# Kernel optimization log

Hardware: AMD Instinct MI355X
Metric: run time of the kernel (lower is better)

Reference implementation:

```python
import jax, jax.numpy as jnp
import numpy as np

N = 100000          # num_nodes
E_TYPES = 5         # num_edge_type
N_EDGES = 500000    # edges per relation type
W_IN = 256
W_OUT = 128         # args.node_dim
C = 2               # args.num_channels
L = 2               # args.num_layers
NUM_CLASS = 3
BETA = 0.1


def _glorot(k, sh):
    lim = np.sqrt(6.0 / (sh[-2] + sh[-1]))
    return jax.random.uniform(k, sh, jnp.float32, -lim, lim)


def setup_inputs() -> dict:
    key = jax.random.key(0)
    ks = jax.random.split(key, 8)
    edge_index = jax.random.randint(ks[0], (E_TYPES, 2, N_EDGES), 0, N)
    edge_value = jax.random.uniform(ks[1], (E_TYPES, N_EDGES), dtype=jnp.float32)
    X = jax.random.normal(ks[2], (N, W_IN), dtype=jnp.float32)
    Ws = _glorot(ks[3], (C, W_IN, W_OUT))                      # GCNConv weights per channel
    conv_w = jax.random.normal(ks[4], (L, C, E_TYPES), dtype=jnp.float32) * 0.1  # FastGTConv weights
    lin1_w = _glorot(ks[5], (C * W_OUT, W_OUT))
    lin1_b = jnp.zeros((W_OUT,), jnp.float32)
    lin2_w = _glorot(ks[6], (W_OUT, NUM_CLASS))
    lin2_b = jnp.zeros((NUM_CLASS,), jnp.float32)
    return dict(edge_index=edge_index, edge_value=edge_value, X=X, Ws=Ws,
                conv_w=conv_w, lin1_w=lin1_w, lin1_b=lin1_b,
                lin2_w=lin2_w, lin2_b=lin2_b, num_nodes=N)


def reference(edge_index, edge_value, X, Ws, conv_w, lin1_w, lin1_b, lin2_w, lin2_b, num_nodes):
    # channel-wise input projections: X_[c] = X @ Ws[c]   -> [C, N, d]
    X_ = jnp.einsum('nf,cfo->cno', X, Ws)
    H = X_
    for l in range(L):
        filt = jax.nn.softmax(conv_w[l], axis=1)  # [C, E] per-channel softmax over edge types
        H_new = jnp.zeros_like(H)
        for j in range(E_TYPES):
            row, col = edge_index[j, 0], edge_index[j, 1]
            # sparse A_j @ H per channel: gather cols, weight by edge value, scatter-add rows
            msg = H[:, col, :] * edge_value[j][None, :, None]          # [C, Ej, d]
            agg = jax.vmap(lambda m: jax.ops.segment_sum(m, row, num_segments=num_nodes))(msg)
            H_new = H_new + filt[:, j][:, None, None] * agg
        # NOTE: source's `H = H + init_H` is Python list concat -> unused entries; no residual.
        H = H_new
    Hrelu = jax.nn.relu(BETA * X_ + (1.0 - BETA) * H)                  # [C, N, d]
    H_ = jnp.concatenate([Hrelu[c] for c in range(C)], axis=1)         # channel_agg='concat'
    H_ = H_ @ lin1_w + lin1_b                                          # [N, d]
    return H_ @ lin2_w + lin2_b                                        # [N, num_class]
```

## Files before the change

### kernel.cpp

```cpp
#include <hip/hip_runtime.h>

#define NN   100000
#define ETY  5
#define NE   500000
#define WIN  256
#define WOUT 128
#define CCH  2
#define LAY  2
#define NCLS 3

#define NTOT   (ETY * NE)
#define BSHIFT 7
#define BNODES 128
#define NBUCK  ((NN + BNODES - 1) / BNODES)
#define BCAP   4096
#define ACHUNK 8192

typedef __attribute__((ext_vector_type(8))) short bf16x8;
typedef __attribute__((ext_vector_type(4))) float f32x4;

__device__ __forceinline__ unsigned short f2bf(float f) {
    union { float f; unsigned u; } v; v.f = f;
    unsigned u = v.u + 0x7FFFu + ((v.u >> 16) & 1u);
    return (unsigned short)(u >> 16);
}
__device__ __forceinline__ float bf2f(unsigned short u) {
    union { unsigned u; float f; } v; v.u = ((unsigned)u) << 16;
    return v.f;
}

__device__ __forceinline__ bf16x8 pack8(float4 a, float4 b) {
    bf16x8 r;
    r[0] = (short)f2bf(a.x); r[1] = (short)f2bf(a.y);
    r[2] = (short)f2bf(a.z); r[3] = (short)f2bf(a.w);
    r[4] = (short)f2bf(b.x); r[5] = (short)f2bf(b.y);
    r[6] = (short)f2bf(b.z); r[7] = (short)f2bf(b.w);
    return r;
}

__global__ void filt_kernel(const float* __restrict__ conv_w, float* __restrict__ filt) {
    int g = threadIdx.x;
    if (g < LAY * CCH) {
        float m = -1e30f;
        for (int j = 0; j < ETY; ++j) m = fmaxf(m, conv_w[g * ETY + j]);
        float e[ETY], s = 0.f;
        for (int j = 0; j < ETY; ++j) { e[j] = __expf(conv_w[g * ETY + j] - m); s += e[j]; }
        float inv = 1.f / s;
        for (int j = 0; j < ETY; ++j) filt[g * ETY + j] = e[j] * inv;
    }
}

__global__ void wconv_kernel(const float* __restrict__ Ws, const float* __restrict__ w1,
                             unsigned short* __restrict__ Wsb, unsigned short* __restrict__ w1b) {
    int i = blockIdx.x * 256 + threadIdx.x;
    if (i < CCH * WOUT * WIN) {
        int c = i / (WOUT * WIN);
        int r = i - c * WOUT * WIN;
        int n = r / WIN;
        int k = r - n * WIN;
        Wsb[i] = f2bf(Ws[((size_t)c * WIN + k) * WOUT + n]);
    }
    if (i < WOUT * (CCH * WOUT)) {
        int n = i / (CCH * WOUT);
        int k = i - n * (CCH * WOUT);
        w1b[i] = f2bf(w1[(size_t)k * WOUT + n]);
    }
}

__global__ void proj_kernel(const float* __restrict__ X, const unsigned short* __restrict__ Wsb,
                            unsigned short* __restrict__ Xpb) {
    const int tid  = threadIdx.x;
    const int lane = tid & 63;
    const int wv   = tid >> 6;
    const int row0 = blockIdx.x * 64 + wv * 16;
    const int ar   = lane & 15;
    const int kg   = lane >> 4;
    int arow = row0 + ar; if (arow >= NN) arow = NN - 1;
    const float* xrow = X + (size_t)arow * WIN + kg * 8;

    f32x4 acc[2][8];
#pragma unroll
    for (int c = 0; c < 2; ++c)
#pragma unroll
        for (int nt = 0; nt < 8; ++nt) acc[c][nt] = (f32x4){0.f, 0.f, 0.f, 0.f};

#pragma unroll
    for (int kk = 0; kk < 8; ++kk) {
        float4 a0 = *(const float4*)(xrow + kk * 32);
        float4 a1 = *(const float4*)(xrow + kk * 32 + 4);
        bf16x8 af = pack8(a0, a1);
#pragma unroll
        for (int c = 0; c < 2; ++c)
#pragma unroll
            for (int nt = 0; nt < 8; ++nt) {
                const bf16x8 bfm = *(const bf16x8*)(Wsb + (size_t)c * WOUT * WIN +
                                                    (size_t)(nt * 16 + ar) * WIN + kk * 32 + kg * 8);
                acc[c][nt] = __builtin_amdgcn_mfma_f32_16x16x32_bf16(af, bfm, acc[c][nt], 0, 0, 0);
            }
    }
#pragma unroll
    for (int nt = 0; nt < 8; ++nt) {
#pragma unroll
        for (int q = 0; q < 4; ++q) {
            int r = row0 + kg * 4 + q;
            if (r < NN) {
                int col = nt * 16 + ar;
                ushort2 w;
                w.x = f2bf(acc[0][nt][q]);
                w.y = f2bf(acc[1][nt][q]);
                *(ushort2*)(Xpb + (size_t)r * (WOUT * CCH) + col * 2) = w;
            }
        }
    }
}

__global__ void __launch_bounds__(256) bucket_kernel(const int* __restrict__ edge_index,
                                                     const float* __restrict__ edge_value,
                                                     int* __restrict__ bcur, int2* __restrict__ rec) {
    __shared__ int hist[NBUCK];
    __shared__ int start_s[NBUCK];
    const int tid = threadIdx.x;
    const int i0 = blockIdx.x * ACHUNK;
    int i1 = i0 + ACHUNK; if (i1 > NTOT) i1 = NTOT;
    for (int t = tid; t < NBUCK; t += 256) hist[t] = 0;
    __syncthreads();
    for (int i = i0 + tid; i < i1; i += 256) {
        int j = i / NE; int e = i - j * NE;
        int row = edge_index[(size_t)j * 2 * NE + e];
        atomicAdd(&hist[row >> BSHIFT], 1);
    }
    __syncthreads();
    for (int t = tid; t < NBUCK; t += 256) {
        int h = hist[t];
        start_s[t] = h ? atomicAdd(&bcur[t], h) : 0;
        hist[t] = 0;
    }
    __syncthreads();
    for (int i = i0 + tid; i < i1; i += 256) {
        int j = i / NE; int e = i - j * NE;
        int row = edge_index[(size_t)j * 2 * NE + e];
        int col = edge_index[(size_t)j * 2 * NE + NE + e];
        int bk = row >> BSHIFT;
        int p = start_s[bk] + atomicAdd(&hist[bk], 1);
        if (p < BCAP)
            rec[(size_t)bk * BCAP + p] =
                make_int2(col | (j << 17) | ((row & (BNODES - 1)) << 20), __float_as_int(edge_value[i]));
    }
}

__global__ void __launch_bounds__(256) sortb_kernel(const int2* __restrict__ rec,
                                                    const int* __restrict__ bcur,
                                                    const float* __restrict__ filt,
                                                    int* __restrict__ colF, float2* __restrict__ wv0F,
                                                    float2* __restrict__ wv1F, int* __restrict__ baseF,
                                                    int* __restrict__ cntF) {
    __shared__ int nh[BNODES];
    __shared__ int nb[BNODES + 1];
    __shared__ int2 srec[BCAP];
    __shared__ float fl[4 * ETY];
    const int b = blockIdx.x;
    const int tid = threadIdx.x;
    int cnt = bcur[b]; if (cnt > BCAP) cnt = BCAP;
    if (tid < BNODES) nh[tid] = 0;
    if (tid < 4 * ETY) fl[tid] = filt[tid];
    __syncthreads();
    const int2* rb = rec + (size_t)b * BCAP;
    for (int k = tid; k < cnt; k += 256) {
        int r = (rb[k].x >> 20) & (BNODES - 1);
        atomicAdd(&nh[r], 1);
    }
    __syncthreads();
    if (tid < BNODES) nb[tid + 1] = nh[tid];
    if (tid == 0) nb[0] = 0;
    __syncthreads();
    for (int off = 1; off < BNODES; off <<= 1) {
        int v = 0;
        if (tid < BNODES) { v = nb[tid + 1]; if (tid + 1 > off) v += nb[tid + 1 - off]; }
        __syncthreads();
        if (tid < BNODES) nb[tid + 1] = v;
        __syncthreads();
    }
    if (tid < BNODES) nh[tid] = 0;
    __syncthreads();
    for (int k = tid; k < cnt; k += 256) {
        int2 R = rb[k];
        int r = (R.x >> 20) & (BNODES - 1);
        int p = nb[r] + atomicAdd(&nh[r], 1);
        srec[p] = R;
    }
    __syncthreads();
    const size_t g0 = (size_t)b * BCAP;
    for (int k = tid; k < cnt; k += 256) {
        int2 R = srec[k];
        int col = R.x & 0x1FFFF;
        int j = (R.x >> 17) & 7;
        float ev = __int_as_float(R.y);
        colF[g0 + k] = col;
        wv0F[g0 + k] = make_float2(fl[j] * ev, fl[ETY + j] * ev);
        wv1F[g0 + k] = make_float2(fl[2 * ETY + j] * ev, fl[3 * ETY + j] * ev);
    }
    if (tid < BNODES) {
        int n = b * BNODES + tid;
        if (n < NN) {
            baseF[n] = (int)(g0 + nb[tid]);
            cntF[n]  = nb[tid + 1] - nb[tid];
        }
    }
}

__global__ void gather_kernel(const unsigned short* __restrict__ Hin, unsigned short* __restrict__ Hnew,
                              const int* __restrict__ base, const int* __restrict__ cnt,
                              const int* __restrict__ colF, const float2* __restrict__ wv) {
    const int lane = threadIdx.x & 63;
    const int wib  = threadIdx.x >> 6;
    int n0 = blockIdx.x * 4 + wib;
    if (n0 >= NN) return;
    const int n = __builtin_amdgcn_readfirstlane(n0);
    const unsigned short* hp = Hin + lane * 4;
    float a0 = 0.f, a1 = 0.f, a2 = 0.f, a3 = 0.f;
    const int kb = __builtin_amdgcn_readfirstlane(base[n]);
    const int ce = __builtin_amdgcn_readfirstlane(cnt[n]);
    const int e = kb + ce;
    for (int k = kb; k < e; k += 8) {
        int cs[8];
#pragma unroll
        for (int u = 0; u < 8; ++u) {
            int ku = k + u;
            cs[u] = colF[ku < e ? ku : e - 1];
        }
        ushort4 vs[8];
#pragma unroll
        for (int u = 0; u < 8; ++u)
            vs[u] = *(const ushort4*)(hp + (size_t)cs[u] * (WOUT * CCH));
        float2 ws[8];
#pragma unroll
        for (int u = 0; u < 8; ++u) {
            int ku = k + u;
            float2 w = wv[ku < e ? ku : e - 1];
            if (ku >= e) { w.x = 0.f; w.y = 0.f; }
            ws[u] = w;
        }
#pragma unroll
        for (int u = 0; u < 8; ++u) {
            a0 = fmaf(ws[u].x, bf2f(vs[u].x), a0);
            a1 = fmaf(ws[u].y, bf2f(vs[u].y), a1);
            a2 = fmaf(ws[u].x, bf2f(vs[u].z), a2);
            a3 = fmaf(ws[u].y, bf2f(vs[u].w), a3);
        }
    }
    ushort4 r4;
    r4.x = f2bf(a0); r4.y = f2bf(a1); r4.z = f2bf(a2); r4.w = f2bf(a3);
    *(ushort4*)(Hnew + (size_t)n * (WOUT * CCH) + lane * 4) = r4;
}

__global__ void lin_kernel(const unsigned short* __restrict__ Xpb, const unsigned short* __restrict__ Hb,
                           const unsigned short* __restrict__ w1b, const float* __restrict__ b1,
                           const float* __restrict__ w2, const float* __restrict__ b2,
                           float* __restrict__ out) {
    const int tid  = threadIdx.x;
    const int lane = tid & 63;
    const int wv   = tid >> 6;
    const int row0 = blockIdx.x * 64 + wv * 16;
    const int ar   = lane & 15;
    const int kg   = lane >> 4;
    int arow = row0 + ar; if (arow >= NN) arow = NN - 1;
    const unsigned short* xr = Xpb + (size_t)arow * (WOUT * CCH);
    const unsigned short* hr = Hb  + (size_t)arow * (WOUT * CCH);

    f32x4 acc[8];
#pragma unroll
    for (int nt = 0; nt < 8; ++nt) acc[nt] = (f32x4){0.f, 0.f, 0.f, 0.f};

    bf16x8 af1s[4];
#pragma unroll
    for (int kk = 0; kk < 4; ++kk) {
        const int d = kk * 32 + kg * 8;
        bf16x8 af0, af1;
#pragma unroll
        for (int t = 0; t < 4; ++t) {
            ushort4 xu = *(const ushort4*)(xr + 2 * d + 4 * t);
            ushort4 hu = *(const ushort4*)(hr + 2 * d + 4 * t);
            float v00 = fmaxf(0.1f * bf2f(xu.x) + 0.9f * bf2f(hu.x), 0.f);
            float v01 = fmaxf(0.1f * bf2f(xu.y) + 0.9f * bf2f(hu.y), 0.f);
            float v10 = fmaxf(0.1f * bf2f(xu.z) + 0.9f * bf2f(hu.z), 0.f);
            float v11 = fmaxf(0.1f * bf2f(xu.w) + 0.9f * bf2f(hu.w), 0.f);
            af0[2 * t]     = (short)f2bf(v00);
            af0[2 * t + 1] = (short)f2bf(v10);
            af1[2 * t]     = (short)f2bf(v01);
            af1[2 * t + 1] = (short)f2bf(v11);
        }
        af1s[kk] = af1;
        const int k0 = kk * 32 + kg * 8;
#pragma unroll
        for (int nt = 0; nt < 8; ++nt) {
            const bf16x8 bfm = *(const bf16x8*)(w1b + (size_t)(nt * 16 + ar) * (CCH * WOUT) + k0);
            acc[nt] = __builtin_amdgcn_mfma_f32_16x16x32_bf16(af0, bfm, acc[nt], 0, 0, 0);
        }
    }
#pragma unroll
    for (int kk = 4; kk < 8; ++kk) {
        const int k0 = kk * 32 + kg * 8;
        const bf16x8 af = af1s[kk - 4];
#pragma unroll
        for (int nt = 0; nt < 8; ++nt) {
            const bf16x8 bfm = *(const bf16x8*)(w1b + (size_t)(nt * 16 + ar) * (CCH * WOUT) + k0);
            acc[nt] = __builtin_amdgcn_mfma_f32_16x16x32_bf16(af, bfm, acc[nt], 0, 0, 0);
        }
    }

    float b1v[8], w2v[8][NCLS];
#pragma unroll
    for (int nt = 0; nt < 8; ++nt) {
        int col = nt * 16 + ar;
        b1v[nt] = b1[col];
#pragma unroll
        for (int m = 0; m < NCLS; ++m) w2v[nt][m] = w2[col * NCLS + m];
    }
#pragma unroll
    for (int q = 0; q < 4; ++q) {
        float pm[NCLS] = {0.f, 0.f, 0.f};
#pragma unroll
        for (int nt = 0; nt < 8; ++nt) {
            float h = acc[nt][q] + b1v[nt];
#pragma unroll
            for (int m = 0; m < NCLS; ++m) pm[m] = fmaf(h, w2v[nt][m], pm[m]);
        }
#pragma unroll
        for (int m = 0; m < NCLS; ++m) {
            pm[m] += __shfl_xor(pm[m], 1);
            pm[m] += __shfl_xor(pm[m], 2);
            pm[m] += __shfl_xor(pm[m], 4);
            pm[m] += __shfl_xor(pm[m], 8);
        }
        int r = row0 + kg * 4 + q;
        if (ar == 0 && r < NN) {
            out[(size_t)r * NCLS + 0] = pm[0] + b2[0];
            out[(size_t)r * NCLS + 1] = pm[1] + b2[1];
            out[(size_t)r * NCLS + 2] = pm[2] + b2[2];
        }
    }
}

extern "C" void kernel_launch(void* const* d_in, const int* in_sizes, int n_in,
                              void* d_out, int out_size, void* d_ws, size_t ws_size,
                              hipStream_t stream) {
    const int*   edge_index = (const int*)d_in[0];
    const float* edge_value = (const float*)d_in[1];
    const float* X          = (const float*)d_in[2];
    const float* Ws         = (const float*)d_in[3];
    const float* conv_w     = (const float*)d_in[4];
    const float* lin1_w     = (const float*)d_in[5];
    const float* lin1_b     = (const float*)d_in[6];
    const float* lin2_w     = (const float*)d_in[7];
    const float* lin2_b     = (const float*)d_in[8];
    float* out = (float*)d_out;

    const size_t CNU  = (size_t)NN * WOUT * CCH;
    const size_t SLOT = (size_t)NBUCK * BCAP;
    unsigned short* Xpb = (unsigned short*)d_ws;
    unsigned short* Ab  = Xpb + CNU;
    unsigned short* Bb  = Ab + CNU;
    float*  filt = (float*)(Bb + CNU);
    int*    bcur = (int*)(filt + 32);
    int*    baseF = bcur + NBUCK;
    int*    cntF  = baseF + NN;
    int2*   rec   = (int2*)(cntF + NN);
    int*    colF  = (int*)(rec + SLOT);
    float2* wv0F  = (float2*)(colF + SLOT);
    float2* wv1F  = wv0F + SLOT;
    unsigned short* Wsb = (unsigned short*)(wv1F + SLOT);
    unsigned short* w1b = Wsb + (size_t)CCH * WOUT * WIN;

    hipMemsetAsync(bcur, 0, NBUCK * sizeof(int), stream);

    filt_kernel<<<1, 64, 0, stream>>>(conv_w, filt);
    wconv_kernel<<<(CCH * WOUT * WIN + 255) / 256, 256, 0, stream>>>(Ws, lin1_w, Wsb, w1b);

    proj_kernel<<<(NN + 63) / 64, 256, 0, stream>>>(X, Wsb, Xpb);

    bucket_kernel<<<(NTOT + ACHUNK - 1) / ACHUNK, 256, 0, stream>>>(edge_index, edge_value, bcur, rec);
    sortb_kernel<<<NBUCK, 256, 0, stream>>>(rec, bcur, filt, colF, wv0F, wv1F, baseF, cntF);

    const int gblocks = (NN + 3) / 4;
    gather_kernel<<<gblocks, 256, 0, stream>>>(Xpb, Ab, baseF, cntF, colF, wv0F);
    gather_kernel<<<gblocks, 256, 0, stream>>>(Ab, Bb, baseF, cntF, colF, wv1F);

    lin_kernel<<<(NN + 63) / 64, 256, 0, stream>>>(Xpb, Bb, w1b, lin1_b, lin2_w, lin2_b, out);
}
```

Baseline: 653.0 us.

## Pack edge column and bf16 weights into one int2 record for gather

Sort output now stores each edge as an int2 holding the column index and two bf16 channel weights, replacing separate column and float2 weight arrays. The gather loop then issues one record load per edge instead of two, which cuts index-stream traffic. The bucket kernel gets a 2D grid indexed by edge type, removing per-element divides, and the filter softmax is folded into the weight-conversion kernel to save a launch. Weights lose precision by being rounded to bf16.

```diff
diff --git a/kernel.cpp b/kernel.cpp
--- a/kernel.cpp
+++ b/kernel.cpp
@@ -15,6 +15,7 @@
 #define NBUCK  ((NN + BNODES - 1) / BNODES)
 #define BCAP   4096
 #define ACHUNK 8192
+#define ABLK   ((NE + ACHUNK - 1) / ACHUNK)
 
 typedef __attribute__((ext_vector_type(8))) short bf16x8;
 typedef __attribute__((ext_vector_type(4))) float f32x4;
@@ -38,9 +39,13 @@
     return r;
 }
 
-__global__ void filt_kernel(const float* __restrict__ conv_w, float* __restrict__ filt) {
-    int g = threadIdx.x;
-    if (g < LAY * CCH) {
+__global__ void wconv_kernel(const float* __restrict__ Ws, const float* __restrict__ w1,
+                             const float* __restrict__ conv_w,
+                             unsigned short* __restrict__ Wsb, unsigned short* __restrict__ w1b,
+                             float* __restrict__ filt) {
+    int i = blockIdx.x * 256 + threadIdx.x;
+    if (i < LAY * CCH) {
+        int g = i;
         float m = -1e30f;
         for (int j = 0; j < ETY; ++j) m = fmaxf(m, conv_w[g * ETY + j]);
         float e[ETY], s = 0.f;
@@ -48,11 +53,6 @@
         float inv = 1.f / s;
         for (int j = 0; j < ETY; ++j) filt[g * ETY + j] = e[j] * inv;
     }
-}
-
-__global__ void wconv_kernel(const float* __restrict__ Ws, const float* __restrict__ w1,
-                             unsigned short* __restrict__ Wsb, unsigned short* __restrict__ w1b) {
-    int i = blockIdx.x * 256 + threadIdx.x;
     if (i < CCH * WOUT * WIN) {
         int c = i / (WOUT * WIN);
         int r = i - c * WOUT * WIN;
@@ -120,15 +120,16 @@
     __shared__ int hist[NBUCK];
     __shared__ int start_s[NBUCK];
     const int tid = threadIdx.x;
+    const int j = blockIdx.y;
     const int i0 = blockIdx.x * ACHUNK;
-    int i1 = i0 + ACHUNK; if (i1 > NTOT) i1 = NTOT;
+    int i1 = i0 + ACHUNK; if (i1 > NE) i1 = NE;
+    const int* rows = edge_index + (size_t)j * 2 * NE;
+    const int* cols = rows + NE;
+    const float* evs = edge_value + (size_t)j * NE;
     for (int t = tid; t < NBUCK; t += 256) hist[t] = 0;
     __syncthreads();
-    for (int i = i0 + tid; i < i1; i += 256) {
-        int j = i / NE; int e = i - j * NE;
-        int row = edge_index[(size_t)j * 2 * NE + e];
-        atomicAdd(&hist[row >> BSHIFT], 1);
-    }
+    for (int i = i0 + tid; i < i1; i += 256)
+        atomicAdd(&hist[rows[i] >> BSHIFT], 1);
     __syncthreads();
     for (int t = tid; t < NBUCK; t += 256) {
         int h = hist[t];
@@ -137,23 +138,21 @@
     }
     __syncthreads();
     for (int i = i0 + tid; i < i1; i += 256) {
-        int j = i / NE; int e = i - j * NE;
-        int row = edge_index[(size_t)j * 2 * NE + e];
-        int col = edge_index[(size_t)j * 2 * NE + NE + e];
+        int row = rows[i];
+        int col = cols[i];
         int bk = row >> BSHIFT;
         int p = start_s[bk] + atomicAdd(&hist[bk], 1);
         if (p < BCAP)
             rec[(size_t)bk * BCAP + p] =
-                make_int2(col | (j << 17) | ((row & (BNODES - 1)) << 20), __float_as_int(edge_value[i]));
+                make_int2(col | (j << 17) | ((row & (BNODES - 1)) << 20), __float_as_int(evs[i]));
     }
 }
 
 __global__ void __launch_bounds__(256) sortb_kernel(const int2* __restrict__ rec,
                                                     const int* __restrict__ bcur,
                                                     const float* __restrict__ filt,
-                                                    int* __restrict__ colF, float2* __restrict__ wv0F,
-                                                    float2* __restrict__ wv1F, int* __restrict__ baseF,
-                                                    int* __restrict__ cntF) {
+                                                    int2* __restrict__ ew0F, int2* __restrict__ ew1F,
+                                                    int* __restrict__ baseF, int* __restrict__ cntF) {
     __shared__ int nh[BNODES];
     __shared__ int nb[BNODES + 1];
     __shared__ int2 srec[BCAP];
@@ -195,9 +194,13 @@
         int col = R.x & 0x1FFFF;
         int j = (R.x >> 17) & 7;
         float ev = __int_as_float(R.y);
-        colF[g0 + k] = col;
-        wv0F[g0 + k] = make_float2(fl[j] * ev, fl[ETY + j] * ev);
-        wv1F[g0 + k] = make_float2(fl[2 * ETY + j] * ev, fl[3 * ETY + j] * ev);
+        int2 E0, E1;
+        E0.x = col;
+        E0.y = (int)((unsigned)f2bf(fl[j] * ev) | ((unsigned)f2bf(fl[ETY + j] * ev) << 16));
+        E1.x = col;
+        E1.y = (int)((unsigned)f2bf(fl[2 * ETY + j] * ev) | ((unsigned)f2bf(fl[3 * ETY + j] * ev) << 16));
+        ew0F[g0 + k] = E0;
+        ew1F[g0 + k] = E1;
     }
     if (tid < BNODES) {
         int n = b * BNODES + tid;
@@ -210,7 +213,7 @@
 
 __global__ void gather_kernel(const unsigned short* __restrict__ Hin, unsigned short* __restrict__ Hnew,
                               const int* __restrict__ base, const int* __restrict__ cnt,
-                              const int* __restrict__ colF, const float2* __restrict__ wv) {
+                              const int2* __restrict__ ewF) {
     const int lane = threadIdx.x & 63;
     const int wib  = threadIdx.x >> 6;
     int n0 = blockIdx.x * 4 + wib;
@@ -222,30 +225,25 @@
     const int ce = __builtin_amdgcn_readfirstlane(cnt[n]);
     const int e = kb + ce;
     for (int k = kb; k < e; k += 8) {
-        int cs[8];
+        int2 es[8];
 #pragma unroll
         for (int u = 0; u < 8; ++u) {
             int ku = k + u;
-            cs[u] = colF[ku < e ? ku : e - 1];
+            es[u] = ewF[ku < e ? ku : e - 1];
         }
         ushort4 vs[8];
 #pragma unroll
         for (int u = 0; u < 8; ++u)
-            vs[u] = *(const ushort4*)(hp + (size_t)cs[u] * (WOUT * CCH));
-        float2 ws[8];
+            vs[u] = *(const ushort4*)(hp + (size_t)es[u].x * (WOUT * CCH));
 #pragma unroll
         for (int u = 0; u < 8; ++u) {
-            int ku = k + u;
-            float2 w = wv[ku < e ? ku : e - 1];
-            if (ku >= e) { w.x = 0.f; w.y = 0.f; }
-            ws[u] = w;
-        }
-#pragma unroll
-        for (int u = 0; u < 8; ++u) {
-            a0 = fmaf(ws[u].x, bf2f(vs[u].x), a0);
-            a1 = fmaf(ws[u].y, bf2f(vs[u].y), a1);
-            a2 = fmaf(ws[u].x, bf2f(vs[u].z), a2);
-            a3 = fmaf(ws[u].y, bf2f(vs[u].w), a3);
+            float w0 = bf2f((unsigned short)(es[u].y & 0xFFFF));
+            float w1 = bf2f((unsigned short)(((unsigned)es[u].y) >> 16));
+            if (k + u >= e) { w0 = 0.f; w1 = 0.f; }
+            a0 = fmaf(w0, bf2f(vs[u].x), a0);
+            a1 = fmaf(w1, bf2f(vs[u].y), a1);
+            a2 = fmaf(w0, bf2f(vs[u].z), a2);
+            a3 = fmaf(w1, bf2f(vs[u].w), a3);
         }
     }
     ushort4 r4;
@@ -360,30 +358,29 @@
     unsigned short* Xpb = (unsigned short*)d_ws;
     unsigned short* Ab  = Xpb + CNU;
     unsigned short* Bb  = Ab + CNU;
-    float*  filt = (float*)(Bb + CNU);
-    int*    bcur = (int*)(filt + 32);
+    float*  filt  = (float*)(Bb + CNU);
+    int*    bcur  = (int*)(filt + 32);
     int*    baseF = bcur + NBUCK;
     int*    cntF  = baseF + NN;
     int2*   rec   = (int2*)(cntF + NN);
-    int*    colF  = (int*)(rec + SLOT);
-    float2* wv0F  = (float2*)(colF + SLOT);
-    float2* wv1F  = wv0F + SLOT;
-    unsigned short* Wsb = (unsigned short*)(wv1F + SLOT);
+    int2*   ew0F  = rec + SLOT;
+    int2*   ew1F  = ew0F + SLOT;
+    unsigned short* Wsb = (unsigned short*)(ew1F + SLOT);
     unsigned short* w1b = Wsb + (size_t)CCH * WOUT * WIN;
 
     hipMemsetAsync(bcur, 0, NBUCK * sizeof(int), stream);
 
-    filt_kernel<<<1, 64, 0, stream>>>(conv_w, filt);
-    wconv_kernel<<<(CCH * WOUT * WIN + 255) / 256, 256, 0, stream>>>(Ws, lin1_w, Wsb, w1b);
+    wconv_kernel<<<(CCH * WOUT * WIN + 255) / 256, 256, 0, stream>>>(Ws, lin1_w, conv_w, Wsb, w1b, filt);
 
     proj_kernel<<<(NN + 63) / 64, 256, 0, stream>>>(X, Wsb, Xpb);
 
-    bucket_kernel<<<(NTOT + ACHUNK - 1) / ACHUNK, 256, 0, stream>>>(edge_index, edge_value, bcur, rec);
-    sortb_kernel<<<NBUCK, 256, 0, stream>>>(rec, bcur, filt, colF, wv0F, wv1F, baseF, cntF);
+    dim3 bg(ABLK, ETY);
+    bucket_kernel<<<bg, 256, 0, stream>>>(edge_index, edge_value, bcur, rec);
+    sortb_kernel<<<NBUCK, 256, 0, stream>>>(rec, bcur, filt, ew0F, ew1F, baseF, cntF);
 
     const int gblocks = (NN + 3) / 4;
-    gather_kernel<<<gblocks, 256, 0, stream>>>(Xpb, Ab, baseF, cntF, colF, wv0F);
-    gather_kernel<<<gblocks, 256, 0, stream>>>(Ab, Bb, baseF, cntF, colF, wv1F);
+    gather_kernel<<<gblocks, 256, 0, stream>>>(Xpb, Ab, baseF, cntF, ew0F);
+    gather_kernel<<<gblocks, 256, 0, stream>>>(Ab, Bb, baseF, cntF, ew1F);
 
     lin_kernel<<<(NN + 63) / 64, 256, 0, stream>>>(Xpb, Bb, w1b, lin1_b, lin2_w, lin2_b, out);
 }
```

New measurement: 641.6 us. About the same (-1.8%).
